# Kernel tuning notes

Measured on AMD Instinct MI355X. Metric: run time of the kernel, lower is better.

## Reference

```python
import jax, jax.numpy as jnp
import numpy as np

D_MODEL = 1024
NUM_HEADS = 16

def setup_inputs() -> dict:
    key = jax.random.key(0)
    k1, k2, k3 = jax.random.split(key, 3)
    scale = 1.0 / np.sqrt(D_MODEL)
    x = jax.random.normal(k1, (2, 2048, D_MODEL), dtype=jnp.float32)
    Wqkv = jax.random.normal(k2, (D_MODEL, 3 * D_MODEL), dtype=jnp.float32) * scale
    bqkv = jnp.zeros((3 * D_MODEL,), dtype=jnp.float32)
    Wout = jax.random.normal(k3, (D_MODEL, D_MODEL), dtype=jnp.float32) * scale
    bout = jnp.zeros((D_MODEL,), dtype=jnp.float32)
    return {"x": x, "Wqkv": Wqkv, "bqkv": bqkv, "Wout": Wout, "bout": bout}

def reference(x, Wqkv, bqkv, Wout, bout):
    B, T, d_model = x.shape
    H = NUM_HEADS
    d_k = d_model // H
    qkv = x @ Wqkv + bqkv                         # [B, T, 3*d_model]
    q, k, v = jnp.split(qkv, 3, axis=-1)
    def reshape(t):
        return t.reshape(B, T, H, d_k).transpose(0, 2, 1, 3)  # [B, H, T, d_k]
    q, k, v = map(reshape, (q, k, v))
    scores = jnp.einsum("bhqd,bhkd->bhqk", q, k) / jnp.sqrt(jnp.float32(d_k))
    attn = jax.nn.softmax(scores, axis=-1)        # [B, H, T, T]
    out = jnp.einsum("bhqk,bhkd->bhqd", attn, v)  # [B, H, T, d_k]
    out = out.transpose(0, 2, 1, 3).reshape(B, T, d_model)
    return out @ Wout + bout
```

## Files before the change

### kernel.cpp

```cpp
#include <hip/hip_runtime.h>
#include <stdint.h>

#define D_MODEL 1024
#define T_SEQ   2048
#define BATCH   2
#define NHEAD   16
#define DK      64

typedef short s16x8 __attribute__((ext_vector_type(8)));
typedef float f32x4 __attribute__((ext_vector_type(4)));
typedef float f32x16 __attribute__((ext_vector_type(16)));

#define MFMA16(a, b, c) __builtin_amdgcn_mfma_f32_16x16x32_bf16((a), (b), (c), 0, 0, 0)
#define MFMA32(a, b, c) __builtin_amdgcn_mfma_f32_32x32x16_bf16((a), (b), (c), 0, 0, 0)
#define CROW(r) ((((r) & 3)) + 8 * ((r) >> 2))

__device__ __forceinline__ unsigned short f2bf(float f) {
    union { float f; unsigned u; } v; v.f = f;
    unsigned r = v.u + 0x7fffu + ((v.u >> 16) & 1u);
    return (unsigned short)(r >> 16);
}

__device__ __forceinline__ unsigned cvtpk_bf16(float lo, float hi) {
    unsigned r;
    asm("v_cvt_pk_bf16_f32 %0, %1, %2" : "=v"(r) : "v"(lo), "v"(hi));
    return r;
}

__device__ __forceinline__ float bperm_f(int srclane, float v) {
    int iv = __builtin_bit_cast(int, v);
    int r = __builtin_amdgcn_ds_bpermute(srclane << 2, iv);
    return __builtin_bit_cast(float, r);
}

__global__ __launch_bounds__(256) void cast_x(const float* __restrict__ in,
                                              unsigned short* __restrict__ out, int n8) {
    int i = blockIdx.x * 256 + threadIdx.x;
    if (i >= n8) return;
    const float4* p = reinterpret_cast<const float4*>(in) + (size_t)i * 2;
    float4 a = p[0], b = p[1];
    union { s16x8 v; unsigned short u[8]; } o;
    o.u[0] = f2bf(a.x); o.u[1] = f2bf(a.y); o.u[2] = f2bf(a.z); o.u[3] = f2bf(a.w);
    o.u[4] = f2bf(b.x); o.u[5] = f2bf(b.y); o.u[6] = f2bf(b.z); o.u[7] = f2bf(b.w);
    reinterpret_cast<s16x8*>(out)[i] = o.v;
}

__global__ __launch_bounds__(256) void transpose_cast(const float* __restrict__ in,
                                                      unsigned short* __restrict__ out,
                                                      int R, int C) {
    __shared__ unsigned short tile[64][66];
    int c0 = blockIdx.x * 64, r0 = blockIdx.y * 64;
    int tid = threadIdx.x;
#pragma unroll
    for (int i = 0; i < 16; ++i) {
        int idx = tid + i * 256;
        int r = idx >> 6, c = idx & 63;
        tile[r][c] = f2bf(in[(size_t)(r0 + r) * C + c0 + c]);
    }
    __syncthreads();
#pragma unroll
    for (int i = 0; i < 16; ++i) {
        int idx = tid + i * 256;
        int cc = idx >> 6, rr = idx & 63;
        out[(size_t)(c0 + cc) * R + r0 + rr] = tile[rr][cc];
    }
}

__global__ __launch_bounds__(256) void transpose_v(const unsigned short* __restrict__ in,
                                                   unsigned short* __restrict__ out) {
    __shared__ unsigned short tile[64][66];
    int t0 = blockIdx.x * 64, bh = blockIdx.y;
    int tid = threadIdx.x;
    const unsigned short* src = in + (size_t)bh * T_SEQ * DK;
    unsigned short* dst = out + (size_t)bh * DK * T_SEQ;
#pragma unroll
    for (int i = 0; i < 16; ++i) {
        int idx = tid + i * 256;
        int tr = idx >> 6, d = idx & 63;
        tile[tr][d] = src[(size_t)(t0 + tr) * DK + d];
    }
    __syncthreads();
#pragma unroll
    for (int i = 0; i < 16; ++i) {
        int idx = tid + i * 256;
        int dd = idx >> 6, tt = idx & 63;
        dst[(size_t)dd * T_SEQ + t0 + tt] = tile[tt][dd];
    }
}

__device__ __forceinline__ void gload_lds16(const void* g, void* l) {
    __builtin_amdgcn_global_load_lds(
        (const __attribute__((address_space(1))) void*)g,
        (__attribute__((address_space(3))) void*)l, 16, 0, 0);
}

template <int EPI>
__global__ __launch_bounds__(256) void gemm_bt(
    const unsigned short* __restrict__ A, const unsigned short* __restrict__ Bt,
    int K, int N, const float* __restrict__ bias,
    float* __restrict__ outF,
    unsigned short* __restrict__ Qw, unsigned short* __restrict__ Kw,
    unsigned short* __restrict__ Vw) {
    __shared__ __align__(16) unsigned short lds[2][8192];
    const int tid = threadIdx.x;
    const int lane = tid & 63, wid = tid >> 6;
    const int g = lane >> 4, l15 = lane & 15;
    const int wm = wid >> 1, wn = wid & 1;
    const int mTile = blockIdx.y, nTile = blockIdx.x;
    const unsigned short* Ab = A + (size_t)mTile * 128 * K;
    const unsigned short* Bb = Bt + (size_t)nTile * 128 * K;
    const int srow = tid >> 2, schunk = (tid & 3) * 8;
    f32x4 acc[4][4] = {};

    auto stage = [&](int buf, int kt) {
        const unsigned short* ga = Ab + (size_t)srow * K + kt * 32 + schunk;
        const unsigned short* gb = Bb + (size_t)srow * K + kt * 32 + schunk;
        unsigned short* la = &lds[buf][tid * 8];
        unsigned short* lb = &lds[buf][4096 + tid * 8];
        gload_lds16(ga, la);
        gload_lds16(ga + (size_t)64 * K, la + 2048);
        gload_lds16(gb, lb);
        gload_lds16(gb + (size_t)64 * K, lb + 2048);
    };

    stage(0, 0);
    __syncthreads();
    const int nk = K >> 5;
    int buf = 0;
    for (int kt = 0; kt < nk; ++kt) {
        if (kt + 1 < nk) stage(buf ^ 1, kt + 1);
        const unsigned short* la = &lds[buf][0];
        const unsigned short* lb = &lds[buf][4096];
        s16x8 af[4], bfr[4];
#pragma unroll
        for (int m = 0; m < 4; ++m)
            af[m] = *(const s16x8*)&la[(wm * 64 + m * 16 + l15) * 32 + g * 8];
#pragma unroll
        for (int n = 0; n < 4; ++n)
            bfr[n] = *(const s16x8*)&lb[(wn * 64 + n * 16 + l15) * 32 + g * 8];
#pragma unroll
        for (int m = 0; m < 4; ++m)
#pragma unroll
            for (int n = 0; n < 4; ++n)
                acc[m][n] = MFMA16(af[m], bfr[n], acc[m][n]);
        __syncthreads();
        buf ^= 1;
    }

    const int rowBase = mTile * 128 + wm * 64;
    const int colBase = nTile * 128 + wn * 64;
#pragma unroll
    for (int m = 0; m < 4; ++m) {
#pragma unroll
        for (int n = 0; n < 4; ++n) {
            int col = colBase + n * 16 + l15;
            float bv = bias[col];
#pragma unroll
            for (int r = 0; r < 4; ++r) {
                int row = rowBase + m * 16 + 4 * g + r;
                float val = acc[m][n][r] + bv;
                if (EPI == 1) {
                    outF[(size_t)row * N + col] = val;
                } else {
                    int b = row >> 11, t = row & 2047;
                    if (col < 1024) {
                        int h = col >> 6, d = col & 63;
                        Qw[(((size_t)(b * NHEAD + h)) * T_SEQ + t) * DK + d] = f2bf(val * 0.125f);
                    } else if (col < 2048) {
                        int h = (col - 1024) >> 6, d = col & 63;
                        Kw[(((size_t)(b * NHEAD + h)) * T_SEQ + t) * DK + d] = f2bf(val);
                    } else {
                        int h = (col - 2048) >> 6, d = col & 63;
                        Vw[(((size_t)(b * NHEAD + h)) * T_SEQ + t) * DK + d] = f2bf(val);
                    }
                }
            }
        }
    }
}

__global__ __launch_bounds__(256) void attn_fwd(
    const unsigned short* __restrict__ Q, const unsigned short* __restrict__ Kx,
    const unsigned short* __restrict__ Vt, unsigned short* __restrict__ O) {
    const int tid = threadIdx.x;
    const int lane = tid & 63, wid = tid >> 6;
    const int l31 = lane & 31, hi = lane >> 5;
    const int bh = blockIdx.y;
    const int b = bh >> 4, h = bh & 15;
    const int q0 = blockIdx.x * 128 + wid * 32;
    const unsigned short* Qh = Q + (size_t)bh * T_SEQ * DK;
    const unsigned short* Kh = Kx + (size_t)bh * T_SEQ * DK;
    const unsigned short* Vh = Vt + (size_t)bh * DK * T_SEQ;

    s16x8 qf[4];
#pragma unroll
    for (int dt = 0; dt < 4; ++dt)
        qf[dt] = *(const s16x8*)&Qh[(size_t)(q0 + l31) * DK + dt * 16 + hi * 8];

    f32x16 o0 = {}, o1 = {};
    float m = -1e30f, lr = 0.f;

    for (int kv0 = 0; kv0 < T_SEQ; kv0 += 64) {
        s16x8 kf[2][4];
#pragma unroll
        for (int kt = 0; kt < 2; ++kt)
#pragma unroll
            for (int dt = 0; dt < 4; ++dt)
                kf[kt][dt] = *(const s16x8*)&Kh[(size_t)(kv0 + kt * 32 + l31) * DK + dt * 16 + hi * 8];
        s16x8 vf[2][4];
#pragma unroll
        for (int dt2 = 0; dt2 < 2; ++dt2)
#pragma unroll
            for (int ks = 0; ks < 4; ++ks)
                vf[dt2][ks] = *(const s16x8*)&Vh[(size_t)(dt2 * 32 + l31) * T_SEQ + kv0 + ks * 16 + hi * 8];

        f32x16 p[2] = {};
#pragma unroll
        for (int kt = 0; kt < 2; ++kt)
#pragma unroll
            for (int dt = 0; dt < 4; ++dt)
                p[kt] = MFMA32(kf[kt][dt], qf[dt], p[kt]);

        float tm = p[0][0];
#pragma unroll
        for (int r = 1; r < 16; ++r) tm = fmaxf(tm, p[0][r]);
#pragma unroll
        for (int r = 0; r < 16; ++r) tm = fmaxf(tm, p[1][r]);
        tm = fmaxf(tm, __shfl_xor(tm, 32));

        if (!__all(tm <= m + 8.0f)) {
            float mn = fmaxf(m, tm);
            float sf = __expf(m - mn);
            lr *= sf;
            m = mn;
            float sfr;
#pragma unroll
            for (int r = 0; r < 16; ++r) {
                sfr = bperm_f(CROW(r) + 4 * hi, sf);
                o0[r] *= sfr; o1[r] *= sfr;
            }
        }

        float ts = 0.f;
#pragma unroll
        for (int kt = 0; kt < 2; ++kt)
#pragma unroll
            for (int r = 0; r < 16; ++r) {
                float e = __expf(p[kt][r] - m);
                p[kt][r] = e;
                ts += e;
            }
        lr += ts;

#pragma unroll
        for (int ks = 0; ks < 4; ++ks) {
            const int kt = ks >> 1, rb = (ks & 1) * 8;
            unsigned w0 = cvtpk_bf16(p[kt][rb + 0], p[kt][rb + 1]);
            unsigned w2 = cvtpk_bf16(p[kt][rb + 4], p[kt][rb + 5]);
            asm volatile("v_permlane32_swap_b32 %0, %1" : "+v"(w0), "+v"(w2));
            unsigned w1 = cvtpk_bf16(p[kt][rb + 2], p[kt][rb + 3]);
            unsigned w3 = cvtpk_bf16(p[kt][rb + 6], p[kt][rb + 7]);
            asm volatile("v_permlane32_swap_b32 %0, %1" : "+v"(w1), "+v"(w3));
            union { unsigned w[4]; s16x8 v; } pu;
            pu.w[0] = w0; pu.w[1] = w1; pu.w[2] = w2; pu.w[3] = w3;
            o0 = MFMA32(pu.v, vf[0][ks], o0);
            o1 = MFMA32(pu.v, vf[1][ks], o1);
        }
    }

    lr += __shfl_xor(lr, 32);
    float li = 1.f / lr;
#pragma unroll
    for (int r = 0; r < 16; ++r) {
        float lir = bperm_f(CROW(r) + 4 * hi, li);
        int q = q0 + CROW(r) + 4 * hi;
        size_t base = ((size_t)(b * T_SEQ + q)) * D_MODEL + h * DK;
        O[base + l31]      = f2bf(o0[r] * lir);
        O[base + 32 + l31] = f2bf(o1[r] * lir);
    }
}

extern "C" void kernel_launch(void* const* d_in, const int* in_sizes, int n_in,
                              void* d_out, int out_size, void* d_ws, size_t ws_size,
                              hipStream_t stream) {
    const float* x    = (const float*)d_in[0];
    const float* Wqkv = (const float*)d_in[1];
    const float* bqkv = (const float*)d_in[2];
    const float* Wout = (const float*)d_in[3];
    const float* bout = (const float*)d_in[4];
    float* out = (float*)d_out;

    char* ws = (char*)d_ws;
    unsigned short* Xbf    = (unsigned short*)(ws + 0);
    unsigned short* WqkvT  = (unsigned short*)(ws + 8388608);
    unsigned short* WoutT  = (unsigned short*)(ws + 14680064);
    unsigned short* Qw     = (unsigned short*)(ws + 16777216);
    unsigned short* Kw     = (unsigned short*)(ws + 25165824);
    unsigned short* Vtmp   = (unsigned short*)(ws + 33554432);
    unsigned short* Vte    = (unsigned short*)(ws + 41943040);
    unsigned short* Ows    = (unsigned short*)(ws + 50331648);

    cast_x<<<2048, 256, 0, stream>>>(x, Xbf, (BATCH * T_SEQ * D_MODEL) / 8);
    transpose_cast<<<dim3(48, 16), 256, 0, stream>>>(Wqkv, WqkvT, 1024, 3072);
    transpose_cast<<<dim3(16, 16), 256, 0, stream>>>(Wout, WoutT, 1024, 1024);
    gemm_bt<0><<<dim3(24, 32), 256, 0, stream>>>(Xbf, WqkvT, 1024, 3072, bqkv,
                                                 nullptr, Qw, Kw, Vtmp);
    transpose_v<<<dim3(32, 32), 256, 0, stream>>>(Vtmp, Vte);
    attn_fwd<<<dim3(16, 32), 256, 0, stream>>>(Qw, Kw, Vte, Ows);
    gemm_bt<1><<<dim3(8, 32), 256, 0, stream>>>(Ows, WoutT, 1024, 1024, bout,
                                                out, nullptr, nullptr, nullptr);
}
```

Baseline: 266.1 us.

## Double-buffer K/V register loads in attention and use exp2 softmax

Restructures the attention inner loop so the next K/V tile is loaded into registers while the current tile is computed, hiding global load latency with a two-buffer ping-pong. Folds log2(e) into the Q scale so softmax can use the raw v_exp_f32 (exp2) instruction instead of __expf. Also turns the max and sum reductions into trees with multiple accumulators to shorten dependency chains, and sets launch_bounds to 2 blocks per CU. The extra register buffer raises register pressure. The last iteration issues a wasted reload of tile 0.

After: 270.3 us. No clear change (+1.5%).

```diff
diff --git a/kernel.cpp b/kernel.cpp
--- a/kernel.cpp
+++ b/kernel.cpp
@@ -24,6 +24,12 @@
 __device__ __forceinline__ unsigned cvtpk_bf16(float lo, float hi) {
     unsigned r;
     asm("v_cvt_pk_bf16_f32 %0, %1, %2" : "=v"(r) : "v"(lo), "v"(hi));
+    return r;
+}
+
+__device__ __forceinline__ float exp2a(float x) {
+    float r;
+    asm("v_exp_f32 %0, %1" : "=v"(r) : "v"(x));
     return r;
 }
 
@@ -165,7 +171,8 @@
                     int b = row >> 11, t = row & 2047;
                     if (col < 1024) {
                         int h = col >> 6, d = col & 63;
-                        Qw[(((size_t)(b * NHEAD + h)) * T_SEQ + t) * DK + d] = f2bf(val * 0.125f);
+                        Qw[(((size_t)(b * NHEAD + h)) * T_SEQ + t) * DK + d] =
+                            f2bf(val * 0.1803368801111137f);
                     } else if (col < 2048) {
                         int h = (col - 1024) >> 6, d = col & 63;
                         Kw[(((size_t)(b * NHEAD + h)) * T_SEQ + t) * DK + d] = f2bf(val);
@@ -179,7 +186,12 @@
     }
 }
 
-__global__ __launch_bounds__(256) void attn_fwd(
+struct KV {
+    s16x8 kf[2][4];
+    s16x8 vf[2][4];
+};
+
+__global__ __launch_bounds__(256, 2) void attn_fwd(
     const unsigned short* __restrict__ Q, const unsigned short* __restrict__ Kx,
     const unsigned short* __restrict__ Vt, unsigned short* __restrict__ O) {
     const int tid = threadIdx.x;
@@ -200,57 +212,64 @@
     f32x16 o0 = {}, o1 = {};
     float m = -1e30f, lr = 0.f;
 
-    for (int kv0 = 0; kv0 < T_SEQ; kv0 += 64) {
-        s16x8 kf[2][4];
+    auto loadKV = [&](int kv0) -> KV {
+        KV kv;
 #pragma unroll
         for (int kt = 0; kt < 2; ++kt)
 #pragma unroll
             for (int dt = 0; dt < 4; ++dt)
-                kf[kt][dt] = *(const s16x8*)&Kh[(size_t)(kv0 + kt * 32 + l31) * DK + dt * 16 + hi * 8];
-        s16x8 vf[2][4];
+                kv.kf[kt][dt] = *(const s16x8*)&Kh[(size_t)(kv0 + kt * 32 + l31) * DK + dt * 16 + hi * 8];
 #pragma unroll
         for (int dt2 = 0; dt2 < 2; ++dt2)
 #pragma unroll
             for (int ks = 0; ks < 4; ++ks)
-                vf[dt2][ks] = *(const s16x8*)&Vh[(size_t)(dt2 * 32 + l31) * T_SEQ + kv0 + ks * 16 + hi * 8];
-
+                kv.vf[dt2][ks] = *(const s16x8*)&Vh[(size_t)(dt2 * 32 + l31) * T_SEQ + kv0 + ks * 16 + hi * 8];
+        return kv;
+    };
+
+    auto computeTile = [&](const KV& kv) {
         f32x16 p[2] = {};
 #pragma unroll
         for (int kt = 0; kt < 2; ++kt)
 #pragma unroll
             for (int dt = 0; dt < 4; ++dt)
-                p[kt] = MFMA32(kf[kt][dt], qf[dt], p[kt]);
-
-        float tm = p[0][0];
-#pragma unroll
-        for (int r = 1; r < 16; ++r) tm = fmaxf(tm, p[0][r]);
-#pragma unroll
-        for (int r = 0; r < 16; ++r) tm = fmaxf(tm, p[1][r]);
+                p[kt] = MFMA32(kv.kf[kt][dt], qf[dt], p[kt]);
+
+        float t16[16];
+#pragma unroll
+        for (int r = 0; r < 16; ++r) t16[r] = fmaxf(p[0][r], p[1][r]);
+#pragma unroll
+        for (int r = 0; r < 8; ++r) t16[r] = fmaxf(t16[r], t16[r + 8]);
+#pragma unroll
+        for (int r = 0; r < 4; ++r) t16[r] = fmaxf(t16[r], t16[r + 4]);
+        float tm = fmaxf(fmaxf(t16[0], t16[1]), fmaxf(t16[2], t16[3]));
         tm = fmaxf(tm, __shfl_xor(tm, 32));
 
         if (!__all(tm <= m + 8.0f)) {
             float mn = fmaxf(m, tm);
-            float sf = __expf(m - mn);
+            float sf = exp2a(m - mn);
             lr *= sf;
             m = mn;
-            float sfr;
 #pragma unroll
             for (int r = 0; r < 16; ++r) {
-                sfr = bperm_f(CROW(r) + 4 * hi, sf);
+                float sfr = bperm_f(CROW(r) + 4 * hi, sf);
                 o0[r] *= sfr; o1[r] *= sfr;
             }
         }
 
-        float ts = 0.f;
+        float ts0 = 0.f, ts1 = 0.f, ts2 = 0.f, ts3 = 0.f;
 #pragma unroll
         for (int kt = 0; kt < 2; ++kt)
 #pragma unroll
             for (int r = 0; r < 16; ++r) {
-                float e = __expf(p[kt][r] - m);
+                float e = exp2a(p[kt][r] - m);
                 p[kt][r] = e;
-                ts += e;
+                if ((r & 3) == 0) ts0 += e;
+                else if ((r & 3) == 1) ts1 += e;
+                else if ((r & 3) == 2) ts2 += e;
+                else ts3 += e;
             }
-        lr += ts;
+        lr += (ts0 + ts1) + (ts2 + ts3);
 
 #pragma unroll
         for (int ks = 0; ks < 4; ++ks) {
@@ -263,9 +282,18 @@
             asm volatile("v_permlane32_swap_b32 %0, %1" : "+v"(w1), "+v"(w3));
             union { unsigned w[4]; s16x8 v; } pu;
             pu.w[0] = w0; pu.w[1] = w1; pu.w[2] = w2; pu.w[3] = w3;
-            o0 = MFMA32(pu.v, vf[0][ks], o0);
-            o1 = MFMA32(pu.v, vf[1][ks], o1);
+            o0 = MFMA32(pu.v, kv.vf[0][ks], o0);
+            o1 = MFMA32(pu.v, kv.vf[1][ks], o1);
         }
+    };
+
+    KV bufA = loadKV(0);
+#pragma unroll 1
+    for (int i = 0; i < 16; ++i) {
+        KV bufB = loadKV((2 * i + 1) * 64);
+        computeTile(bufA);
+        bufA = loadKV(((2 * i + 2) & 31) * 64);
+        computeTile(bufB);
     }
 
     lr += __shfl_xor(lr, 32);
```
